# Performance work log

Hardware: AMD Instinct MI355X
Metric: run time of the kernel (lower is better)

Reference implementation:

```python
import jax, jax.numpy as jnp
import numpy as np

N_NODES = 100000
N_EDGES = 1600000
IN_F, HID_F, OUT_F = 256, 128, 32


def spmm(rows, cols, vals, x):
    # out[i] = sum_{e: rows[e]==i} vals[e] * x[cols[e]]  -- COO SpMM
    msgs = vals[:, None] * x[cols]            # [E, F] gathered weighted messages
    return jax.ops.segment_sum(msgs, rows, num_segments=N_NODES)


def setup_inputs() -> dict:
    key = jax.random.key(0)
    k = jax.random.split(key, 6)
    x = jax.random.normal(k[0], (N_NODES, IN_F), dtype=jnp.float32)
    adj_rows = jax.random.randint(k[1], (N_EDGES,), 0, N_NODES, dtype=jnp.int32)
    adj_cols = jax.random.randint(k[2], (N_EDGES,), 0, N_NODES, dtype=jnp.int32)
    adj_vals = jax.random.uniform(k[3], (N_EDGES,), dtype=jnp.float32)
    W1 = jax.random.normal(k[4], (IN_F, HID_F), dtype=jnp.float32) / np.sqrt(IN_F)
    W2 = jax.random.normal(k[5], (HID_F, OUT_F), dtype=jnp.float32) / np.sqrt(HID_F)
    return {"x": x, "adj_rows": adj_rows, "adj_cols": adj_cols,
            "adj_vals": adj_vals, "W1": W1, "W2": W2}


def reference(x, adj_rows, adj_cols, adj_vals, W1, W2):
    # TwoLayerGCN forward (eval mode: dropout = identity, labels=None)
    h = spmm(adj_rows, adj_cols, adj_vals, x @ W1)   # conv1: linear then A_hat @
    h = jax.nn.relu(h)
    out = spmm(adj_rows, adj_cols, adj_vals, h @ W2)  # conv2
    return out
```

## Files before the change

### kernel.cpp

```cpp
#include <hip/hip_runtime.h>
#include <hip/hip_bf16.h>

#define N_NODES 100000
#define IN_F 256
#define HID_F 128
#define OUT_F 32
#define NBUCK 391
#define BCAP  5120
#define ACHUNK 4096
#define NCHUNKS ((1600000 + ACHUNK - 1) / ACHUNK)

typedef __bf16 bf16x8 __attribute__((ext_vector_type(8)));
typedef __bf16 bf16x2 __attribute__((ext_vector_type(2)));
typedef float  f32x4  __attribute__((ext_vector_type(4)));

__global__ void cvt_w1t_kernel(const float* __restrict__ W1, __bf16* __restrict__ W1T) {
    int i = blockIdx.x * 256 + threadIdx.x;
    if (i >= IN_F * HID_F) return;
    int n = i >> 8, k = i & 255;
    W1T[i] = (__bf16)W1[k * HID_F + n];
}

__device__ __forceinline__
void bucketize_body(char* smem, int blk,
                    const int* __restrict__ rows, const int* __restrict__ cols,
                    const float* __restrict__ vals, int* __restrict__ gcnt,
                    int2* __restrict__ staged, int E) {
    int2* lcv  = (int2*)smem;
    int* lcnt  = (int*)(smem + ACHUNK * 8);
    int* loff  = lcnt + NBUCK;
    int* lcur  = loff + NBUCK;
    int* gbase = lcur + NBUCK;
    int* psum  = gbase + NBUCK;

    const int t    = threadIdx.x;
    const int base = blk * ACHUNK;

    for (int b = t; b < NBUCK; b += 256) lcnt[b] = 0;
    __syncthreads();

    int myrow[16];
#pragma unroll
    for (int i = 0; i < 16; ++i) {
        int e = base + t + i * 256;
        int r = (e < E) ? rows[e] : -1;
        myrow[i] = r;
        if (r >= 0) atomicAdd(&lcnt[r >> 8], 1);
    }
    __syncthreads();

    int s0 = (t * 2     < NBUCK) ? lcnt[t * 2]     : 0;
    int s1 = (t * 2 + 1 < NBUCK) ? lcnt[t * 2 + 1] : 0;
    int local = s0 + s1;
    psum[t] = local;
    __syncthreads();
    for (int off = 1; off < 256; off <<= 1) {
        int v = (t >= off) ? psum[t - off] : 0;
        __syncthreads();
        psum[t] += v;
        __syncthreads();
    }
    int excl = psum[t] - local;
    if (t * 2     < NBUCK) { loff[t * 2]     = excl;      lcur[t * 2]     = excl; }
    if (t * 2 + 1 < NBUCK) { loff[t * 2 + 1] = excl + s0; lcur[t * 2 + 1] = excl + s0; }
    __syncthreads();

#pragma unroll
    for (int i = 0; i < 16; ++i) {
        int r = myrow[i];
        if (r >= 0) {
            int e = base + t + i * 256;
            int posl = atomicAdd(&lcur[r >> 8], 1);
            lcv[posl] = make_int2(cols[e] | ((r & 255) << 20), __float_as_int(vals[e]));
        }
    }
    __syncthreads();

    for (int b = t; b < NBUCK; b += 256) {
        int c = lcnt[b];
        gbase[b] = c ? atomicAdd(&gcnt[b], c) : 0;
    }
    __syncthreads();

    int total = loff[NBUCK - 1] + lcnt[NBUCK - 1];
    for (int i = t; i < total; i += 256) {
        int lo = 0, hi = NBUCK - 1;
        while (lo < hi) {
            int mid = (lo + hi + 1) >> 1;
            if (loff[mid] <= i) lo = mid; else hi = mid - 1;
        }
        int idx = gbase[lo] + (i - loff[lo]);
        if (idx < BCAP)
            staged[(size_t)lo * BCAP + idx] = lcv[i];
    }
}

__device__ __forceinline__
void gemm1_body(char* smem, int blk,
                const float* __restrict__ x, const __bf16* __restrict__ W1T,
                __bf16* __restrict__ xw) {
    __bf16 (*Xs)[76] = (__bf16 (*)[76])smem;
    __bf16 (*Bs)[76] = (__bf16 (*)[76])(smem + 19456);

    const int r0   = blk * 128;
    const int t    = threadIdx.x;
    const int wv   = t >> 6;
    const int lane = t & 63;
    const int quad = lane >> 4;
    const int l15  = lane & 15;

    f32x4 acc[2][8];
#pragma unroll
    for (int rt = 0; rt < 2; ++rt)
#pragma unroll
        for (int nt = 0; nt < 8; ++nt)
            acc[rt][nt] = (f32x4){0.f, 0.f, 0.f, 0.f};

    const int srow = t >> 3;
    const int soct = t & 7;

    for (int q = 0; q < 4; ++q) {
        const int kq = q * 64;
#pragma unroll
        for (int j = 0; j < 4; ++j) {
            int row = j * 32 + srow;
            int gm = r0 + row;
            if (gm > N_NODES - 1) gm = N_NODES - 1;
            const float* xp = x + (size_t)gm * IN_F + kq + soct * 8;
            float4 f0 = *(const float4*)xp;
            float4 f1 = *(const float4*)(xp + 4);
            bf16x8 v = { (__bf16)f0.x, (__bf16)f0.y, (__bf16)f0.z, (__bf16)f0.w,
                         (__bf16)f1.x, (__bf16)f1.y, (__bf16)f1.z, (__bf16)f1.w };
            *(bf16x8*)(&Xs[row][soct * 8]) = v;
        }
#pragma unroll
        for (int i = 0; i < 4; ++i) {
            int idx = t + i * 256;
            int n = idx >> 3, kc = idx & 7;
            bf16x8 w = *(const bf16x8*)(W1T + n * 256 + kq + kc * 8);
            *(bf16x8*)(&Bs[n][kc * 8]) = w;
        }
        __syncthreads();

#pragma unroll
        for (int kt = 0; kt < 2; ++kt) {
            const int k0 = kt * 32;
            bf16x8 a[2];
#pragma unroll
            for (int rt = 0; rt < 2; ++rt)
                a[rt] = *(const bf16x8*)(&Xs[wv * 32 + rt * 16 + l15][k0 + quad * 8]);
            bf16x8 b[8];
#pragma unroll
            for (int nt = 0; nt < 8; ++nt)
                b[nt] = *(const bf16x8*)(&Bs[nt * 16 + l15][k0 + quad * 8]);
#pragma unroll
            for (int rt = 0; rt < 2; ++rt)
#pragma unroll
                for (int nt = 0; nt < 8; ++nt)
                    acc[rt][nt] = __builtin_amdgcn_mfma_f32_16x16x32_bf16(
                        a[rt], b[nt], acc[rt][nt], 0, 0, 0);
        }
        __syncthreads();
    }

#pragma unroll
    for (int rt = 0; rt < 2; ++rt)
#pragma unroll
        for (int nt = 0; nt < 8; ++nt)
#pragma unroll
            for (int reg = 0; reg < 4; ++reg) {
                int row = r0 + wv * 32 + rt * 16 + quad * 4 + reg;
                if (row < N_NODES)
                    xw[(size_t)row * HID_F + nt * 16 + l15] = (__bf16)acc[rt][nt][reg];
            }
}

__global__ __launch_bounds__(256, 4)
void fused_gemm1_bucketize_kernel(const float* __restrict__ x,
                                  const __bf16* __restrict__ W1T,
                                  __bf16* __restrict__ xw,
                                  const int* __restrict__ rows,
                                  const int* __restrict__ cols,
                                  const float* __restrict__ vals,
                                  int* __restrict__ gcnt,
                                  int2* __restrict__ staged, int E) {
    __shared__ __align__(16) char smem[40448];
    if (blockIdx.x < NCHUNKS)
        bucketize_body(smem, blockIdx.x, rows, cols, vals, gcnt, staged, E);
    else
        gemm1_body(smem, blockIdx.x - NCHUNKS, x, W1T, xw);
}

__global__ __launch_bounds__(256)
void bucket_csr_kernel(const int* __restrict__ gcnt,
                       const int2* __restrict__ staged,
                       int* __restrict__ row_ptr, int2* __restrict__ pedge) {
    __shared__ int2 lcv[BCAP];
    __shared__ int lcnt[256], loff[256], lcur[256];
    __shared__ int psum[256];
    __shared__ int boff[NBUCK + 1];

    const int b = blockIdx.x;
    const int t = threadIdx.x;

    int c0 = (t * 2     < NBUCK) ? min(gcnt[t * 2],     BCAP) : 0;
    int c1 = (t * 2 + 1 < NBUCK) ? min(gcnt[t * 2 + 1], BCAP) : 0;
    int local = c0 + c1;
    psum[t] = local;
    __syncthreads();
    for (int off = 1; off < 256; off <<= 1) {
        int v = (t >= off) ? psum[t - off] : 0;
        __syncthreads();
        psum[t] += v;
        __syncthreads();
    }
    int excl = psum[t] - local;
    if (t * 2     < NBUCK)  boff[t * 2]     = excl;
    if (t * 2 + 1 <= NBUCK) boff[t * 2 + 1] = excl + c0;
    __syncthreads();

    int n = gcnt[b]; if (n > BCAP) n = BCAP;
    const int2* sp = staged + (size_t)b * BCAP;
    const int base = boff[b];

    if (b == NBUCK - 1 && t == 0) row_ptr[N_NODES] = boff[NBUCK];

    lcnt[t] = 0;
    __syncthreads();
    for (int i = t; i < n; i += 256) {
        int2 v = sp[i];
        lcv[i] = v;
        atomicAdd(&lcnt[(v.x >> 20) & 255], 1);
    }
    __syncthreads();

    int v = lcnt[t];
    loff[t] = v;
    __syncthreads();
    for (int off = 1; off < 256; off <<= 1) {
        int u = (t >= off) ? loff[t - off] : 0;
        __syncthreads();
        loff[t] += u;
        __syncthreads();
    }
    int excl2 = loff[t] - v;
    lcur[t] = excl2;
    __syncthreads();

    int row = (b << 8) + t;
    if (row < N_NODES) row_ptr[row] = base + excl2;

    for (int i = t; i < n; i += 256) {
        int2 cv = lcv[i];
        int r = (cv.x >> 20) & 255;
        int pos = atomicAdd(&lcur[r], 1);
        pedge[base + pos] = make_int2(cv.x & 0xFFFFF, cv.y);
    }
}

__global__ __launch_bounds__(256)
void gemm2_mfma_kernel(const __bf16* __restrict__ h,
                       const float* __restrict__ W2,
                       __bf16* __restrict__ hw) {
    const int r0   = blockIdx.x * 128;
    const int wv   = threadIdx.x >> 6;
    const int lane = threadIdx.x & 63;
    const int quad = lane >> 4;
    const int l15  = lane & 15;

    __shared__ __bf16 W2T[32][136];

    for (int i = threadIdx.x; i < 32 * 128; i += 256) {
        int n = i & 31, k = i >> 5;
        W2T[n][k] = (__bf16)W2[k * OUT_F + n];
    }
    __syncthreads();

    f32x4 acc[2][2];
#pragma unroll
    for (int rt = 0; rt < 2; ++rt)
#pragma unroll
        for (int nt = 0; nt < 2; ++nt)
            acc[rt][nt] = (f32x4){0.f, 0.f, 0.f, 0.f};

#pragma unroll
    for (int kt = 0; kt < 4; ++kt) {
        const int k0 = kt * 32;
        bf16x8 a[2];
#pragma unroll
        for (int rt = 0; rt < 2; ++rt) {
            int gm = r0 + wv * 32 + rt * 16 + l15;
            if (gm > N_NODES - 1) gm = N_NODES - 1;
            a[rt] = *(const bf16x8*)(h + (size_t)gm * HID_F + k0 + quad * 8);
        }
        bf16x8 b[2];
#pragma unroll
        for (int nt = 0; nt < 2; ++nt)
            b[nt] = *(const bf16x8*)(&W2T[nt * 16 + l15][k0 + quad * 8]);
#pragma unroll
        for (int rt = 0; rt < 2; ++rt)
#pragma unroll
            for (int nt = 0; nt < 2; ++nt)
                acc[rt][nt] = __builtin_amdgcn_mfma_f32_16x16x32_bf16(
                    a[rt], b[nt], acc[rt][nt], 0, 0, 0);
    }

#pragma unroll
    for (int rt = 0; rt < 2; ++rt)
#pragma unroll
        for (int nt = 0; nt < 2; ++nt)
#pragma unroll
            for (int reg = 0; reg < 4; ++reg) {
                int row = r0 + wv * 32 + rt * 16 + quad * 4 + reg;
                if (row < N_NODES)
                    hw[(size_t)row * OUT_F + nt * 16 + l15] = (__bf16)acc[rt][nt][reg];
            }
}

__global__ __launch_bounds__(256)
void spmm1_kernel(const int* __restrict__ row_ptr,
                  const int2* __restrict__ pedge,
                  const __bf16* __restrict__ src,
                  __bf16* __restrict__ dst) {
    int row = __builtin_amdgcn_readfirstlane(blockIdx.x * 4 + (threadIdx.x >> 6));
    int lane = threadIdx.x & 63;
    if (row >= N_NODES) return;

    const int e0 = row_ptr[row];
    const int e1 = row_ptr[row + 1];

    float a0 = 0.f, a1 = 0.f;
    for (int e = e0; e < e1; e += 8) {
        int2 p[8];
#pragma unroll
        for (int j = 0; j < 8; ++j) {
            int ee = e + j;
            if (ee >= e1) ee = e1 - 1;
            p[j] = pedge[ee];
            if (e + j >= e1) p[j].y = 0;
        }
        bf16x2 s[8];
#pragma unroll
        for (int j = 0; j < 8; ++j)
            s[j] = ((const bf16x2*)(src + (size_t)p[j].x * HID_F))[lane];
#pragma unroll
        for (int j = 0; j < 8; ++j) {
            float v = __int_as_float(p[j].y);
            a0 += v * (float)s[j].x;
            a1 += v * (float)s[j].y;
        }
    }
    a0 = fmaxf(a0, 0.f);
    a1 = fmaxf(a1, 0.f);
    bf16x2 o = { (__bf16)a0, (__bf16)a1 };
    ((bf16x2*)(dst + (size_t)row * HID_F))[lane] = o;
}

__global__ __launch_bounds__(256)
void spmm2_kernel(const int* __restrict__ row_ptr,
                  const int2* __restrict__ pedge,
                  const __bf16* __restrict__ src,
                  float* __restrict__ dst) {
    long long gid = (long long)blockIdx.x * 256 + threadIdx.x;
    int row  = (int)(gid >> 4);
    int lane = (int)(gid & 15);
    if (row >= N_NODES) return;

    const int e0 = row_ptr[row];
    const int e1 = row_ptr[row + 1];

    float a0 = 0.f, a1 = 0.f;
    for (int e = e0; e < e1; e += 8) {
        int2 p[8];
#pragma unroll
        for (int j = 0; j < 8; ++j) {
            int ee = e + j;
            if (ee >= e1) ee = e1 - 1;
            p[j] = pedge[ee];
            if (e + j >= e1) p[j].y = 0;
        }
        bf16x2 s[8];
#pragma unroll
        for (int j = 0; j < 8; ++j)
            s[j] = ((const bf16x2*)(src + (size_t)p[j].x * OUT_F))[lane];
#pragma unroll
        for (int j = 0; j < 8; ++j) {
            float v = __int_as_float(p[j].y);
            a0 += v * (float)s[j].x;
            a1 += v * (float)s[j].y;
        }
    }
    ((float2*)(dst + (size_t)row * OUT_F))[lane] = make_float2(a0, a1);
}

extern "C" void kernel_launch(void* const* d_in, const int* in_sizes, int n_in,
                              void* d_out, int out_size, void* d_ws, size_t ws_size,
                              hipStream_t stream) {
    const float* x        = (const float*)d_in[0];
    const int*   adj_rows = (const int*)d_in[1];
    const int*   adj_cols = (const int*)d_in[2];
    const float* adj_vals = (const float*)d_in[3];
    const float* W1       = (const float*)d_in[4];
    const float* W2       = (const float*)d_in[5];
    float*       out      = (float*)d_out;
    const int E = in_sizes[1];

    char* p = (char*)d_ws;
    __bf16* W1T  = (__bf16*)p;  p += (size_t)IN_F * HID_F * sizeof(__bf16);
    __bf16* xw   = (__bf16*)p;  p += (size_t)N_NODES * HID_F * sizeof(__bf16);
    __bf16* h    = (__bf16*)p;  p += (size_t)N_NODES * HID_F * sizeof(__bf16);
    __bf16* hw   = (__bf16*)p;  p += (size_t)N_NODES * OUT_F * sizeof(__bf16);
    int*   row_ptr = (int*)p;   p += (size_t)(N_NODES + 1) * sizeof(int);
    int*   gcnt    = (int*)p;   p += ((NBUCK + 255) & ~255) * sizeof(int);
    p = (char*)(((uintptr_t)p + 15) & ~(uintptr_t)15);
    int2*  pedge   = (int2*)p;  p += (size_t)E * sizeof(int2);
    p = (char*)(((uintptr_t)p + 15) & ~(uintptr_t)15);
    int2*  staged  = (int2*)p;  p += (size_t)NBUCK * BCAP * sizeof(int2);

    hipMemsetAsync(gcnt, 0, (size_t)NBUCK * sizeof(int), stream);
    cvt_w1t_kernel<<<(IN_F * HID_F + 255) / 256, 256, 0, stream>>>(W1, W1T);

    fused_gemm1_bucketize_kernel<<<NCHUNKS + (N_NODES + 127) / 128, 256, 0, stream>>>(
        x, W1T, xw, adj_rows, adj_cols, adj_vals, gcnt, staged, E);

    bucket_csr_kernel<<<NBUCK, 256, 0, stream>>>(gcnt, staged, row_ptr, pedge);

    spmm1_kernel<<<(N_NODES + 3) / 4, 256, 0, stream>>>(row_ptr, pedge, xw, h);

    gemm2_mfma_kernel<<<(N_NODES + 127) / 128, 256, 0, stream>>>(h, W2, hw);
    {
        long long threads = (long long)N_NODES * 16;
        spmm2_kernel<<<(int)((threads + 255) / 256), 256, 0, stream>>>(
            row_ptr, pedge, hw, out);
    }
}
```

Before: 312.8 us.

## Split fused gemm1/bucketize kernel and stage gemm1 output through LDS

Splits the fused kernel, which branched on block index between bucketizing edges and the first GEMM, back into two separate kernels launched one after the other. Each kernel now declares only the shared memory it needs. The GEMM epilogue now writes the accumulators into an LDS tile and then issues coalesced 16-byte row stores to xw, replacing the scattered 2-byte stores. This trades the concurrency of running both jobs in one launch for better occupancy and store efficiency in each kernel, at the cost of an extra launch and a barrier in the epilogue.

```diff
diff --git a/kernel.cpp b/kernel.cpp
--- a/kernel.cpp
+++ b/kernel.cpp
@@ -21,11 +21,11 @@
     W1T[i] = (__bf16)W1[k * HID_F + n];
 }
 
-__device__ __forceinline__
-void bucketize_body(char* smem, int blk,
-                    const int* __restrict__ rows, const int* __restrict__ cols,
-                    const float* __restrict__ vals, int* __restrict__ gcnt,
-                    int2* __restrict__ staged, int E) {
+__global__ __launch_bounds__(256)
+void bucketize_kernel(const int* __restrict__ rows, const int* __restrict__ cols,
+                      const float* __restrict__ vals, int* __restrict__ gcnt,
+                      int2* __restrict__ staged, int E) {
+    __shared__ __align__(16) char smem[40048];
     int2* lcv  = (int2*)smem;
     int* lcnt  = (int*)(smem + ACHUNK * 8);
     int* loff  = lcnt + NBUCK;
@@ -34,7 +34,7 @@
     int* psum  = gbase + NBUCK;
 
     const int t    = threadIdx.x;
-    const int base = blk * ACHUNK;
+    const int base = blockIdx.x * ACHUNK;
 
     for (int b = t; b < NBUCK; b += 256) lcnt[b] = 0;
     __syncthreads();
@@ -95,14 +95,15 @@
     }
 }
 
-__device__ __forceinline__
-void gemm1_body(char* smem, int blk,
-                const float* __restrict__ x, const __bf16* __restrict__ W1T,
-                __bf16* __restrict__ xw) {
+__global__ __launch_bounds__(256, 4)
+void gemm1_kernel(const float* __restrict__ x, const __bf16* __restrict__ W1T,
+                  __bf16* __restrict__ xw) {
+    __shared__ __align__(16) char smem[38912];
     __bf16 (*Xs)[76] = (__bf16 (*)[76])smem;
     __bf16 (*Bs)[76] = (__bf16 (*)[76])(smem + 19456);
-
-    const int r0   = blk * 128;
+    __bf16 (*Ls)[136] = (__bf16 (*)[136])smem;
+
+    const int r0   = blockIdx.x * 128;
     const int t    = threadIdx.x;
     const int wv   = t >> 6;
     const int lane = t & 63;
@@ -168,27 +169,21 @@
 #pragma unroll
         for (int nt = 0; nt < 8; ++nt)
 #pragma unroll
-            for (int reg = 0; reg < 4; ++reg) {
-                int row = r0 + wv * 32 + rt * 16 + quad * 4 + reg;
-                if (row < N_NODES)
-                    xw[(size_t)row * HID_F + nt * 16 + l15] = (__bf16)acc[rt][nt][reg];
-            }
-}
-
-__global__ __launch_bounds__(256, 4)
-void fused_gemm1_bucketize_kernel(const float* __restrict__ x,
-                                  const __bf16* __restrict__ W1T,
-                                  __bf16* __restrict__ xw,
-                                  const int* __restrict__ rows,
-                                  const int* __restrict__ cols,
-                                  const float* __restrict__ vals,
-                                  int* __restrict__ gcnt,
-                                  int2* __restrict__ staged, int E) {
-    __shared__ __align__(16) char smem[40448];
-    if (blockIdx.x < NCHUNKS)
-        bucketize_body(smem, blockIdx.x, rows, cols, vals, gcnt, staged, E);
-    else
-        gemm1_body(smem, blockIdx.x - NCHUNKS, x, W1T, xw);
+            for (int reg = 0; reg < 4; ++reg)
+                Ls[wv * 32 + rt * 16 + quad * 4 + reg][nt * 16 + l15] =
+                    (__bf16)acc[rt][nt][reg];
+    __syncthreads();
+
+#pragma unroll
+    for (int i = 0; i < 8; ++i) {
+        int id = i * 256 + t;
+        int row = id >> 4, cc = id & 15;
+        int g = r0 + row;
+        if (g < N_NODES) {
+            bf16x8 v = *(const bf16x8*)(&Ls[row][cc * 8]);
+            *(bf16x8*)(xw + (size_t)g * HID_F + cc * 8) = v;
+        }
+    }
 }
 
 __global__ __launch_bounds__(256)
@@ -420,8 +415,9 @@
     hipMemsetAsync(gcnt, 0, (size_t)NBUCK * sizeof(int), stream);
     cvt_w1t_kernel<<<(IN_F * HID_F + 255) / 256, 256, 0, stream>>>(W1, W1T);
 
-    fused_gemm1_bucketize_kernel<<<NCHUNKS + (N_NODES + 127) / 128, 256, 0, stream>>>(
-        x, W1T, xw, adj_rows, adj_cols, adj_vals, gcnt, staged, E);
+    bucketize_kernel<<<NCHUNKS, 256, 0, stream>>>(
+        adj_rows, adj_cols, adj_vals, gcnt, staged, E);
+    gemm1_kernel<<<(N_NODES + 127) / 128, 256, 0, stream>>>(x, W1T, xw);
 
     bucket_csr_kernel<<<NBUCK, 256, 0, stream>>>(gcnt, staged, row_ptr, pedge);
 
```

After: 341.3 us. +9.1%, slower.
